# Performance work log

Hardware: AMD Instinct MI355X
Metric: run time of the kernel (lower is better)

The kernel has to match this reference:

```python
import jax, jax.numpy as jnp
import numpy as np

B, N, F, UNITS = 8, 4096, 128, 64
NEG = -1e10
LEAKY_SLOPE = 0.2  # tf.nn.leaky_relu default


def setup_inputs() -> dict:
    key = jax.random.key(0)
    k1, k2, k3, k4, k5 = jax.random.split(key, 5)
    H = jax.random.normal(k1, (B, N, F), dtype=jnp.float32)
    A = jax.random.randint(k2, (B, N, N), 0, 2).astype(jnp.float32)
    # self-loops so every row has at least one unmasked entry
    A = jnp.maximum(A, jnp.eye(N, dtype=jnp.float32)[None])
    W = jax.random.normal(k3, (F, UNITS), dtype=jnp.float32) * (1.0 / np.sqrt(F))
    a_1 = jax.random.normal(k4, (UNITS, 1), dtype=jnp.float32) * (1.0 / np.sqrt(UNITS))
    a_2 = jax.random.normal(k5, (UNITS, 1), dtype=jnp.float32) * (1.0 / np.sqrt(UNITS))
    return {"H": H, "A": A, "W": W, "a_1": a_1, "a_2": a_2}


def reference(H, A, W, a_1, a_2):
    X = H @ W                                  # [B, N, U]
    attn_self = X @ a_1                        # [B, N, 1]
    attn_neigh = X @ a_2                       # [B, N, 1]
    attention = attn_self + jnp.swapaxes(attn_neigh, 1, 2)   # [B, N, N]
    E = jax.nn.leaky_relu(attention, negative_slope=LEAKY_SLOPE)
    masked_E = E + NEG * (1.0 - A)
    alpha = jax.nn.softmax(masked_E, axis=-1)  # row-wise softmax
    H_cap = alpha @ X                          # [B, N, U]
    return jax.nn.relu(H_cap)
```

## Files before the change

kernel.cpp:

```cpp
#include <hip/hip_runtime.h>
#include <hip/hip_bf16.h>


#define NTOK 4096
#define FDIM 128
#define UDIM 64
#define BATCH 8
#define BK 64

typedef __attribute__((ext_vector_type(8))) short short8;
typedef __attribute__((ext_vector_type(4))) float f32x4;

union PackU { unsigned u[4]; short8 s; };

__device__ __forceinline__ unsigned short f2bf(float x) {
    unsigned u = __float_as_uint(x);
    return (unsigned short)((u + 0x7fffu + ((u >> 16) & 1u)) >> 16);
}

__global__ __launch_bounds__(256) void prep_kernel(
    const float* __restrict__ H,
    const float* __restrict__ W,
    const float* __restrict__ a1,
    const float* __restrict__ a2,
    unsigned short* __restrict__ XT,
    float* __restrict__ s_out,
    float* __restrict__ t_out)
{
    __shared__ float Xl[4][16][UDIM + 1];

    const int tid  = threadIdx.x;
    const int wave = tid >> 6, lane = tid & 63;
    const int col  = lane & 15, quad = lane >> 4;
    const int i0   = (blockIdx.x * 4 + wave) * 16;

    f32x4 acc0 = {0,0,0,0}, acc1 = {0,0,0,0}, acc2 = {0,0,0,0}, acc3 = {0,0,0,0};
    const float* hrow = H + (size_t)(i0 + col) * FDIM + quad * 8;

    #pragma unroll
    for (int kb = 0; kb < FDIM; kb += 32) {
        f32x4 h0 = *(const f32x4*)(hrow + kb);
        f32x4 h1 = *(const f32x4*)(hrow + kb + 4);
        short8 afr, b0, b1, b2, b3;
        #pragma unroll
        for (int j = 0; j < 4; ++j) {
            afr[j]     = (short)f2bf(h0[j]);
            afr[4 + j] = (short)f2bf(h1[j]);
        }
        #pragma unroll
        for (int j = 0; j < 8; ++j) {
            int k = kb + quad * 8 + j;
            b0[j] = (short)f2bf(W[k * UDIM + col]);
            b1[j] = (short)f2bf(W[k * UDIM + 16 + col]);
            b2[j] = (short)f2bf(W[k * UDIM + 32 + col]);
            b3[j] = (short)f2bf(W[k * UDIM + 48 + col]);
        }
        acc0 = __builtin_amdgcn_mfma_f32_16x16x32_bf16(afr, b0, acc0, 0, 0, 0);
        acc1 = __builtin_amdgcn_mfma_f32_16x16x32_bf16(afr, b1, acc1, 0, 0, 0);
        acc2 = __builtin_amdgcn_mfma_f32_16x16x32_bf16(afr, b2, acc2, 0, 0, 0);
        acc3 = __builtin_amdgcn_mfma_f32_16x16x32_bf16(afr, b3, acc3, 0, 0, 0);
    }
    #pragma unroll
    for (int r = 0; r < 4; ++r) {
        Xl[wave][quad * 4 + r][col]      = acc0[r];
        Xl[wave][quad * 4 + r][16 + col] = acc1[r];
        Xl[wave][quad * 4 + r][32 + col] = acc2[r];
        Xl[wave][quad * 4 + r][48 + col] = acc3[r];
    }
    __syncthreads();

    const int b = i0 >> 12, n0 = i0 & (NTOK - 1);
    float ps = 0.f, pt = 0.f;
    #pragma unroll
    for (int ui = 0; ui < 16; ++ui) {
        int u = quad * 16 + ui;
        float x = Xl[wave][col][u];
        ps = fmaf(x, a1[u], ps);
        pt = fmaf(x, a2[u], pt);
    }
    ps += __shfl_xor(ps, 16, 64); ps += __shfl_xor(ps, 32, 64);
    pt += __shfl_xor(pt, 16, 64); pt += __shfl_xor(pt, 32, 64);
    const float LOG2E = 1.44269504f;
    if (quad == 0) s_out[i0 + col] = ps * LOG2E;
    if (quad == 1) t_out[i0 + col] = pt * LOG2E;

    #pragma unroll
    for (int ui = 0; ui < 16; ++ui) {
        int u = quad * 16 + ui;
        XT[(size_t)(b * UDIM + u) * NTOK + n0 + col] = f2bf(Xl[wave][col][u]);
    }
}

__global__ __launch_bounds__(256) void attn_kernel(
    const float* __restrict__ A,
    const unsigned short* __restrict__ XT,
    const float* __restrict__ s_in,
    const float* __restrict__ t_in,
    float* __restrict__ out)
{
    __shared__ __align__(16) float          As[2][64][BK + 4];
    __shared__ __align__(16) unsigned short Xs[2][64][BK + 8];

    const int tid  = threadIdx.x;
    const int wave = tid >> 6, lane = tid & 63;
    const int col  = lane & 15, quad = lane >> 4;
    const int b    = blockIdx.x & 7;
    const int i0   = (blockIdx.x >> 3) * 64;

    const int arow = tid >> 4, acol = (tid & 15) * 4;
    const int xrow = tid >> 3, xcol = (tid & 7) * 8;
    const float* agp = A + ((size_t)(b * NTOK + i0 + arow)) * NTOK + acol;
    const unsigned short* xgp = XT + ((size_t)(b * UDIM + xrow)) * NTOK + xcol;

    const float s_m = s_in[b * NTOK + i0 + wave * 16 + col];
    const float* tbase = t_in + b * NTOK;

    f32x4 acc[4];
    #pragma unroll
    for (int f = 0; f < 4; ++f) acc[f] = (f32x4){0,0,0,0};
    float den = 0.f;

    f32x4 av[4], xv[2];

    #pragma unroll
    for (int i = 0; i < 4; ++i)
        av[i] = __builtin_nontemporal_load((const f32x4*)(agp + (size_t)i * 16 * NTOK));
    #pragma unroll
    for (int i = 0; i < 2; ++i)
        xv[i] = *(const f32x4*)(xgp + (size_t)i * 32 * NTOK);
    #pragma unroll
    for (int i = 0; i < 4; ++i) *(f32x4*)&As[0][arow + i * 16][acol] = av[i];
    #pragma unroll
    for (int i = 0; i < 2; ++i) *(f32x4*)&Xs[0][xrow + i * 32][xcol] = xv[i];

    for (int c = 0; c < NTOK / BK; ++c) {
        const int buf = c & 1;
        if (c < NTOK / BK - 1) {
            const float* ag = agp + (c + 1) * BK;
            const unsigned short* xg = xgp + (c + 1) * BK;
            #pragma unroll
            for (int i = 0; i < 4; ++i)
                av[i] = __builtin_nontemporal_load((const f32x4*)(ag + (size_t)i * 16 * NTOK));
            #pragma unroll
            for (int i = 0; i < 2; ++i)
                xv[i] = *(const f32x4*)(xg + (size_t)i * 32 * NTOK);
        }
        __syncthreads();

        #pragma unroll
        for (int ks = 0; ks < 2; ++ks) {
            const float* ar = &As[buf][wave * 16 + col][ks * 32 + quad * 8];
            f32x4 a0 = *(const f32x4*)ar;
            f32x4 a1 = *(const f32x4*)(ar + 4);
            const float* tp = tbase + c * BK + ks * 32 + quad * 8;
            f32x4 t0 = *(const f32x4*)tp;
            f32x4 t1 = *(const f32x4*)(tp + 4);

            unsigned uw[8];
            #pragma unroll
            for (int j = 0; j < 4; ++j) {
                float l0 = s_m + t0[j], l1 = s_m + t1[j];
                float e0 = fmaxf(l0, 0.2f * l0);
                float e1 = fmaxf(l1, 0.2f * l1);
                float w0 = __builtin_amdgcn_exp2f(e0) * a0[j];
                float w1 = __builtin_amdgcn_exp2f(e1) * a1[j];
                den += w0 + w1;
                uw[j]     = __float_as_uint(w0) + 0x8000u;
                uw[4 + j] = __float_as_uint(w1) + 0x8000u;
            }
            PackU p;
            p.u[0] = __builtin_amdgcn_perm(uw[1], uw[0], 0x07060302u);
            p.u[1] = __builtin_amdgcn_perm(uw[3], uw[2], 0x07060302u);
            p.u[2] = __builtin_amdgcn_perm(uw[5], uw[4], 0x07060302u);
            p.u[3] = __builtin_amdgcn_perm(uw[7], uw[6], 0x07060302u);

            short8 bf0 = *(const short8*)&Xs[buf][col]     [ks * 32 + quad * 8];
            short8 bf1 = *(const short8*)&Xs[buf][16 + col][ks * 32 + quad * 8];
            short8 bf2 = *(const short8*)&Xs[buf][32 + col][ks * 32 + quad * 8];
            short8 bf3 = *(const short8*)&Xs[buf][48 + col][ks * 32 + quad * 8];

            acc[0] = __builtin_amdgcn_mfma_f32_16x16x32_bf16(p.s, bf0, acc[0], 0, 0, 0);
            acc[1] = __builtin_amdgcn_mfma_f32_16x16x32_bf16(p.s, bf1, acc[1], 0, 0, 0);
            acc[2] = __builtin_amdgcn_mfma_f32_16x16x32_bf16(p.s, bf2, acc[2], 0, 0, 0);
            acc[3] = __builtin_amdgcn_mfma_f32_16x16x32_bf16(p.s, bf3, acc[3], 0, 0, 0);
        }

        if (c < NTOK / BK - 1) {
            const int nb = buf ^ 1;
            #pragma unroll
            for (int i = 0; i < 4; ++i) *(f32x4*)&As[nb][arow + i * 16][acol] = av[i];
            #pragma unroll
            for (int i = 0; i < 2; ++i) *(f32x4*)&Xs[nb][xrow + i * 32][xcol] = xv[i];
        }
    }

    den += __shfl_xor(den, 16, 64);
    den += __shfl_xor(den, 32, 64);
    #pragma unroll
    for (int r = 0; r < 4; ++r) {
        float dd = __shfl(den, quad * 4 + r, 64);
        const int row = i0 + wave * 16 + quad * 4 + r;
        #pragma unroll
        for (int f = 0; f < 4; ++f) {
            float o = fmaxf(acc[f][r] / dd, 0.f);
            __builtin_nontemporal_store(o, &out[(size_t)(b * NTOK + row) * UDIM + f * 16 + col]);
        }
    }
}

extern "C" void kernel_launch(void* const* d_in, const int* in_sizes, int n_in,
                              void* d_out, int out_size, void* d_ws, size_t ws_size,
                              hipStream_t stream) {
    const float* H  = (const float*)d_in[0];
    const float* A  = (const float*)d_in[1];
    const float* W  = (const float*)d_in[2];
    const float* a1 = (const float*)d_in[3];
    const float* a2 = (const float*)d_in[4];
    float* out = (float*)d_out;

    char* ws = (char*)d_ws;
    unsigned short* XT = (unsigned short*)ws;
    size_t off = (size_t)BATCH * UDIM * NTOK * 2;
    float* s = (float*)(ws + off);
    off += (size_t)BATCH * NTOK * 4;
    float* t = (float*)(ws + off);

    prep_kernel<<<512, 256, 0, stream>>>(H, W, a1, a2, XT, s, t);
    attn_kernel<<<512, 256, 0, stream>>>(A, XT, s, t, out);
}
```

Baseline: 702.4 us.

## Stage A, X and t tiles via direct global-to-LDS loads with XOR swizzle

Replaces the register-staged double buffer (global load into VGPRs, then an LDS store) with global_load_lds direct copies into LDS. The LDS tiles switch from padded rows to an XOR-swizzled layout to avoid bank conflicts, and the t vector is now staged through LDS as well. Explicit vmcnt waits and barriers manage the pipeline. This is meant to cut VGPR pressure and LDS store instructions in a kernel bound by streaming A, at the cost of an extra barrier per chunk and the loss of the nontemporal hint on A.

```diff
diff --git a/kernel.cpp b/kernel.cpp
--- a/kernel.cpp
+++ b/kernel.cpp
@@ -7,6 +7,7 @@
 #define UDIM 64
 #define BATCH 8
 #define BK 64
+#define NCHUNK (NTOK / BK)
 
 typedef __attribute__((ext_vector_type(8))) short short8;
 typedef __attribute__((ext_vector_type(4))) float f32x4;
@@ -16,6 +17,17 @@
 __device__ __forceinline__ unsigned short f2bf(float x) {
     unsigned u = __float_as_uint(x);
     return (unsigned short)((u + 0x7fffu + ((u >> 16) & 1u)) >> 16);
+}
+
+__device__ __forceinline__ void gl2lds16(const void* g, void* l) {
+    __builtin_amdgcn_global_load_lds(
+        (const __attribute__((address_space(1))) unsigned int*)g,
+        (__attribute__((address_space(3))) unsigned int*)l, 16, 0, 0);
+}
+__device__ __forceinline__ void gl2lds4(const void* g, void* l) {
+    __builtin_amdgcn_global_load_lds(
+        (const __attribute__((address_space(1))) unsigned int*)g,
+        (__attribute__((address_space(3))) unsigned int*)l, 4, 0, 0);
 }
 
 __global__ __launch_bounds__(256) void prep_kernel(
@@ -98,8 +110,9 @@
     const float* __restrict__ t_in,
     float* __restrict__ out)
 {
-    __shared__ __align__(16) float          As[2][64][BK + 4];
-    __shared__ __align__(16) unsigned short Xs[2][64][BK + 8];
+    __shared__ __align__(16) float          As[2][64 * BK];
+    __shared__ __align__(16) unsigned short Xs[2][64 * BK];
+    __shared__ __align__(16) float          Ts[2][4][BK];
 
     const int tid  = threadIdx.x;
     const int wave = tid >> 6, lane = tid & 63;
@@ -107,54 +120,66 @@
     const int b    = blockIdx.x & 7;
     const int i0   = (blockIdx.x >> 3) * 64;
 
-    const int arow = tid >> 4, acol = (tid & 15) * 4;
-    const int xrow = tid >> 3, xcol = (tid & 7) * 8;
-    const float* agp = A + ((size_t)(b * NTOK + i0 + arow)) * NTOK + acol;
-    const unsigned short* xgp = XT + ((size_t)(b * UDIM + xrow)) * NTOK + xcol;
+    const float* agp[4];
+    #pragma unroll
+    for (int j = 0; j < 4; ++j) {
+        int r = wave * 16 + j * 4 + (lane >> 4);
+        int v = (lane & 15) ^ (r & 7);
+        agp[j] = A + ((size_t)(b * NTOK + i0 + r)) * NTOK + v * 4;
+    }
+    const unsigned short* xgp[2];
+    #pragma unroll
+    for (int j = 0; j < 2; ++j) {
+        int u = wave * 16 + j * 8 + (lane >> 3);
+        int v = (lane & 7) ^ (u & 7);
+        xgp[j] = XT + ((size_t)(b * UDIM + u)) * NTOK + v * 8;
+    }
+    const float* tgp = t_in + b * NTOK + lane;
 
     const float s_m = s_in[b * NTOK + i0 + wave * 16 + col];
-    const float* tbase = t_in + b * NTOK;
 
     f32x4 acc[4];
     #pragma unroll
     for (int f = 0; f < 4; ++f) acc[f] = (f32x4){0,0,0,0};
     float den = 0.f;
 
-    f32x4 av[4], xv[2];
-
-    #pragma unroll
-    for (int i = 0; i < 4; ++i)
-        av[i] = __builtin_nontemporal_load((const f32x4*)(agp + (size_t)i * 16 * NTOK));
-    #pragma unroll
-    for (int i = 0; i < 2; ++i)
-        xv[i] = *(const f32x4*)(xgp + (size_t)i * 32 * NTOK);
-    #pragma unroll
-    for (int i = 0; i < 4; ++i) *(f32x4*)&As[0][arow + i * 16][acol] = av[i];
-    #pragma unroll
-    for (int i = 0; i < 2; ++i) *(f32x4*)&Xs[0][xrow + i * 32][xcol] = xv[i];
-
-    for (int c = 0; c < NTOK / BK; ++c) {
+    #define STAGE(bufi, cc) do {                                              \
+        gl2lds16(agp[0] + (cc) * BK, (void*)&As[bufi][(wave * 4 + 0) * 256]); \
+        gl2lds16(agp[1] + (cc) * BK, (void*)&As[bufi][(wave * 4 + 1) * 256]); \
+        gl2lds16(agp[2] + (cc) * BK, (void*)&As[bufi][(wave * 4 + 2) * 256]); \
+        gl2lds16(agp[3] + (cc) * BK, (void*)&As[bufi][(wave * 4 + 3) * 256]); \
+        gl2lds16(xgp[0] + (cc) * BK, (void*)&Xs[bufi][(wave * 2 + 0) * 512]); \
+        gl2lds16(xgp[1] + (cc) * BK, (void*)&Xs[bufi][(wave * 2 + 1) * 512]); \
+        gl2lds4 (tgp    + (cc) * BK, (void*)&Ts[bufi][wave][0]);              \
+    } while (0)
+
+    STAGE(0, 0);
+    asm volatile("s_waitcnt vmcnt(0)" ::: "memory");
+    __builtin_amdgcn_s_barrier();
+    __builtin_amdgcn_sched_barrier(0);
+
+    #pragma unroll 2
+    for (int c = 0; c < NCHUNK; ++c) {
         const int buf = c & 1;
-        if (c < NTOK / BK - 1) {
-            const float* ag = agp + (c + 1) * BK;
-            const unsigned short* xg = xgp + (c + 1) * BK;
-            #pragma unroll
-            for (int i = 0; i < 4; ++i)
-                av[i] = __builtin_nontemporal_load((const f32x4*)(ag + (size_t)i * 16 * NTOK));
-            #pragma unroll
-            for (int i = 0; i < 2; ++i)
-                xv[i] = *(const f32x4*)(xg + (size_t)i * 32 * NTOK);
-        }
-        __syncthreads();
-
+        if (c + 1 < NCHUNK) {
+            STAGE(buf ^ 1, c + 1);
+            asm volatile("s_waitcnt vmcnt(7)" ::: "memory");
+        } else {
+            asm volatile("s_waitcnt vmcnt(0)" ::: "memory");
+        }
+        __builtin_amdgcn_sched_barrier(0);
+        __builtin_amdgcn_s_barrier();
+        __builtin_amdgcn_sched_barrier(0);
+
+        const int R   = wave * 16 + col;
+        const int xsw = col & 7;
         #pragma unroll
         for (int ks = 0; ks < 2; ++ks) {
-            const float* ar = &As[buf][wave * 16 + col][ks * 32 + quad * 8];
-            f32x4 a0 = *(const f32x4*)ar;
-            f32x4 a1 = *(const f32x4*)(ar + 4);
-            const float* tp = tbase + c * BK + ks * 32 + quad * 8;
-            f32x4 t0 = *(const f32x4*)tp;
-            f32x4 t1 = *(const f32x4*)(tp + 4);
+            const int v0 = 8 * ks + 2 * quad;
+            f32x4 a0 = *(const f32x4*)&As[buf][R * 64 + ((v0)     ^ (R & 7)) * 4];
+            f32x4 a1 = *(const f32x4*)&As[buf][R * 64 + ((v0 + 1) ^ (R & 7)) * 4];
+            f32x4 t0 = *(const f32x4*)&Ts[buf][wave][ks * 32 + quad * 8];
+            f32x4 t1 = *(const f32x4*)&Ts[buf][wave][ks * 32 + quad * 8 + 4];
 
             unsigned uw[8];
             #pragma unroll
@@ -174,25 +199,22 @@
             p.u[2] = __builtin_amdgcn_perm(uw[5], uw[4], 0x07060302u);
             p.u[3] = __builtin_amdgcn_perm(uw[7], uw[6], 0x07060302u);
 
-            short8 bf0 = *(const short8*)&Xs[buf][col]     [ks * 32 + quad * 8];
-            short8 bf1 = *(const short8*)&Xs[buf][16 + col][ks * 32 + quad * 8];
-            short8 bf2 = *(const short8*)&Xs[buf][32 + col][ks * 32 + quad * 8];
-            short8 bf3 = *(const short8*)&Xs[buf][48 + col][ks * 32 + quad * 8];
+            const int xv = (4 * ks + quad) ^ xsw;
+            short8 bf0 = *(const short8*)&Xs[buf][(col)      * 64 + xv * 8];
+            short8 bf1 = *(const short8*)&Xs[buf][(16 + col) * 64 + xv * 8];
+            short8 bf2 = *(const short8*)&Xs[buf][(32 + col) * 64 + xv * 8];
+            short8 bf3 = *(const short8*)&Xs[buf][(48 + col) * 64 + xv * 8];
 
             acc[0] = __builtin_amdgcn_mfma_f32_16x16x32_bf16(p.s, bf0, acc[0], 0, 0, 0);
             acc[1] = __builtin_amdgcn_mfma_f32_16x16x32_bf16(p.s, bf1, acc[1], 0, 0, 0);
             acc[2] = __builtin_amdgcn_mfma_f32_16x16x32_bf16(p.s, bf2, acc[2], 0, 0, 0);
             acc[3] = __builtin_amdgcn_mfma_f32_16x16x32_bf16(p.s, bf3, acc[3], 0, 0, 0);
         }
-
-        if (c < NTOK / BK - 1) {
-            const int nb = buf ^ 1;
-            #pragma unroll
-            for (int i = 0; i < 4; ++i) *(f32x4*)&As[nb][arow + i * 16][acol] = av[i];
-            #pragma unroll
-            for (int i = 0; i < 2; ++i) *(f32x4*)&Xs[nb][xrow + i * 32][xcol] = xv[i];
-        }
-    }
+        __builtin_amdgcn_sched_barrier(0);
+        __builtin_amdgcn_s_barrier();
+        __builtin_amdgcn_sched_barrier(0);
+    }
+    #undef STAGE
 
     den += __shfl_xor(den, 16, 64);
     den += __shfl_xor(den, 32, 64);
```

After: 719.9 us. +2.5%, slower.

## Restructure attention kernel: stage bf16 weights in LDS, split K across waves

Applied to the files above, without the earlier changes.

The attention kernel now uses 512-thread blocks over 32 rows. Each wave streams 4 full rows of A with wide coalesced loads, computes the masked exp weights once, and stores them as bf16 in a double-buffered LDS tile of 512 columns. The MFMA step reads X directly from global/L2 instead of staging it in LDS, and splits the K dimension across four wave groups, with a final LDS reduction and a per-row denominator reduction through shuffles. The aim is better coalescing of the dominant A stream, fewer barriers per byte, and more blocks in flight. In exchange, each block re-reads X from cache and adds a cross-wave reduction.

```diff
diff --git a/kernel.cpp b/kernel.cpp
--- a/kernel.cpp
+++ b/kernel.cpp
@@ -6,7 +6,8 @@
 #define FDIM 128
 #define UDIM 64
 #define BATCH 8
-#define BK 64
+#define CK 512
+#define NCH (NTOK / CK)
 
 typedef __attribute__((ext_vector_type(8))) short short8;
 typedef __attribute__((ext_vector_type(4))) float f32x4;
@@ -91,120 +92,143 @@
     }
 }
 
-__global__ __launch_bounds__(256) void attn_kernel(
+__global__ __launch_bounds__(512, 4) void attn_kernel(
     const float* __restrict__ A,
     const unsigned short* __restrict__ XT,
     const float* __restrict__ s_in,
     const float* __restrict__ t_in,
     float* __restrict__ out)
 {
-    __shared__ __align__(16) float          As[2][64][BK + 4];
-    __shared__ __align__(16) unsigned short Xs[2][64][BK + 8];
+    __shared__ __align__(16) unsigned short Ws[2][32][CK + 8];
+    __shared__ float denl[32];
 
     const int tid  = threadIdx.x;
     const int wave = tid >> 6, lane = tid & 63;
     const int col  = lane & 15, quad = lane >> 4;
     const int b    = blockIdx.x & 7;
-    const int i0   = (blockIdx.x >> 3) * 64;
-
-    const int arow = tid >> 4, acol = (tid & 15) * 4;
-    const int xrow = tid >> 3, xcol = (tid & 7) * 8;
-    const float* agp = A + ((size_t)(b * NTOK + i0 + arow)) * NTOK + acol;
-    const unsigned short* xgp = XT + ((size_t)(b * UDIM + xrow)) * NTOK + xcol;
-
-    const float s_m = s_in[b * NTOK + i0 + wave * 16 + col];
-    const float* tbase = t_in + b * NTOK;
+    const int i0   = (blockIdx.x >> 3) * 32;
+
+    const int g = wave & 1, h = wave >> 1;
+    const int r0 = wave * 4;
+
+    const float* ab = A + ((size_t)(b * NTOK + i0 + r0)) * NTOK + lane * 8;
+    const float* tb = t_in + b * NTOK + lane * 8;
+    float s_r[4];
+    #pragma unroll
+    for (int rr = 0; rr < 4; ++rr) s_r[rr] = s_in[b * NTOK + i0 + r0 + rr];
+
+    const unsigned short* xp[4];
+    #pragma unroll
+    for (int f = 0; f < 4; ++f)
+        xp[f] = XT + ((size_t)(b * UDIM + f * 16 + col)) * NTOK + h * 128 + quad * 8;
 
     f32x4 acc[4];
     #pragma unroll
     for (int f = 0; f < 4; ++f) acc[f] = (f32x4){0,0,0,0};
-    float den = 0.f;
-
-    f32x4 av[4], xv[2];
-
-    #pragma unroll
-    for (int i = 0; i < 4; ++i)
-        av[i] = __builtin_nontemporal_load((const f32x4*)(agp + (size_t)i * 16 * NTOK));
-    #pragma unroll
-    for (int i = 0; i < 2; ++i)
-        xv[i] = *(const f32x4*)(xgp + (size_t)i * 32 * NTOK);
-    #pragma unroll
-    for (int i = 0; i < 4; ++i) *(f32x4*)&As[0][arow + i * 16][acol] = av[i];
-    #pragma unroll
-    for (int i = 0; i < 2; ++i) *(f32x4*)&Xs[0][xrow + i * 32][xcol] = xv[i];
-
-    for (int c = 0; c < NTOK / BK; ++c) {
+    float den_a[4] = {0.f, 0.f, 0.f, 0.f};
+
+    f32x4 av0[4], av1[4], tv0, tv1;
+
+    #define SLOAD(cc) do {                                                         \
+        tv0 = *(const f32x4*)(tb + (cc) * CK);                                     \
+        tv1 = *(const f32x4*)(tb + (cc) * CK + 4);                                 \
+        _Pragma("unroll")                                                          \
+        for (int rr = 0; rr < 4; ++rr) {                                           \
+            av0[rr] = __builtin_nontemporal_load(                                  \
+                (const f32x4*)(ab + (size_t)rr * NTOK + (cc) * CK));               \
+            av1[rr] = __builtin_nontemporal_load(                                  \
+                (const f32x4*)(ab + (size_t)rr * NTOK + (cc) * CK + 4));           \
+        }                                                                          \
+    } while (0)
+
+    #define SWRITE(bufi) do {                                                      \
+        _Pragma("unroll")                                                          \
+        for (int rr = 0; rr < 4; ++rr) {                                           \
+            unsigned uw[8];                                                        \
+            float ds = 0.f;                                                        \
+            _Pragma("unroll")                                                      \
+            for (int j = 0; j < 4; ++j) {                                          \
+                float l0 = s_r[rr] + tv0[j], l1 = s_r[rr] + tv1[j];                \
+                float e0 = fmaxf(l0, 0.2f * l0);               \
+                float e1 = fmaxf(l1, 0.2f * l1);                                   \
+                float w0 = __builtin_amdgcn_exp2f(e0) * av0[rr][j];                \
+                float w1 = __builtin_amdgcn_exp2f(e1) * av1[rr][j];                \
+                ds += w0 + w1;                                                     \
+                uw[j]     = __float_as_uint(w0) + 0x8000u;                         \
+                uw[4 + j] = __float_as_uint(w1) + 0x8000u;                         \
+            }                                                                      \
+            den_a[rr] += ds;                                                       \
+            PackU p;                                                               \
+            p.u[0] = __builtin_amdgcn_perm(uw[1], uw[0], 0x07060302u);             \
+            p.u[1] = __builtin_amdgcn_perm(uw[3], uw[2], 0x07060302u);             \
+            p.u[2] = __builtin_amdgcn_perm(uw[5], uw[4], 0x07060302u);             \
+            p.u[3] = __builtin_amdgcn_perm(uw[7], uw[6], 0x07060302u);             \
+            *(short8*)&Ws[bufi][r0 + rr][lane * 8] = p.s;                          \
+        }                                                                          \
+    } while (0)
+
+    SLOAD(0);
+    SWRITE(0);
+    __syncthreads();
+
+    for (int c = 0; c < NCH; ++c) {
         const int buf = c & 1;
-        if (c < NTOK / BK - 1) {
-            const float* ag = agp + (c + 1) * BK;
-            const unsigned short* xg = xgp + (c + 1) * BK;
+        if (c + 1 < NCH) SLOAD(c + 1);
+
+        const unsigned short* wrow = &Ws[buf][g * 16 + col][h * 128 + quad * 8];
+        #pragma unroll
+        for (int ks = 0; ks < 4; ++ks) {
+            short8 af = *(const short8*)(wrow + ks * 32);
+            short8 b0 = *(const short8*)(xp[0] + c * CK + ks * 32);
+            short8 b1 = *(const short8*)(xp[1] + c * CK + ks * 32);
+            short8 b2 = *(const short8*)(xp[2] + c * CK + ks * 32);
+            short8 b3 = *(const short8*)(xp[3] + c * CK + ks * 32);
+            acc[0] = __builtin_amdgcn_mfma_f32_16x16x32_bf16(af, b0, acc[0], 0, 0, 0);
+            acc[1] = __builtin_amdgcn_mfma_f32_16x16x32_bf16(af, b1, acc[1], 0, 0, 0);
+            acc[2] = __builtin_amdgcn_mfma_f32_16x16x32_bf16(af, b2, acc[2], 0, 0, 0);
+            acc[3] = __builtin_amdgcn_mfma_f32_16x16x32_bf16(af, b3, acc[3], 0, 0, 0);
+        }
+
+        if (c + 1 < NCH) SWRITE(buf ^ 1);
+        __syncthreads();
+    }
+    #undef SLOAD
+    #undef SWRITE
+
+    #pragma unroll
+    for (int rr = 0; rr < 4; ++rr) {
+        float v = den_a[rr];
+        v += __shfl_xor(v, 1, 64);  v += __shfl_xor(v, 2, 64);
+        v += __shfl_xor(v, 4, 64);  v += __shfl_xor(v, 8, 64);
+        v += __shfl_xor(v, 16, 64); v += __shfl_xor(v, 32, 64);
+        if (lane == 0) denl[r0 + rr] = v;
+    }
+    __syncthreads();
+
+    float* red = (float*)&Ws[0][0][0];
+    if (h > 0) {
+        #pragma unroll
+        for (int f = 0; f < 4; ++f)
             #pragma unroll
-            for (int i = 0; i < 4; ++i)
-                av[i] = __builtin_nontemporal_load((const f32x4*)(ag + (size_t)i * 16 * NTOK));
+            for (int r = 0; r < 4; ++r)
+                red[(((h - 1) * 2 + g) * 16 + quad * 4 + r) * 68 + f * 16 + col] = acc[f][r];
+    }
+    __syncthreads();
+    if (h == 0) {
+        #pragma unroll
+        for (int f = 0; f < 4; ++f)
             #pragma unroll
-            for (int i = 0; i < 2; ++i)
-                xv[i] = *(const f32x4*)(xg + (size_t)i * 32 * NTOK);
-        }
-        __syncthreads();
-
-        #pragma unroll
-        for (int ks = 0; ks < 2; ++ks) {
-            const float* ar = &As[buf][wave * 16 + col][ks * 32 + quad * 8];
-            f32x4 a0 = *(const f32x4*)ar;
-            f32x4 a1 = *(const f32x4*)(ar + 4);
-            const float* tp = tbase + c * BK + ks * 32 + quad * 8;
-            f32x4 t0 = *(const f32x4*)tp;
-            f32x4 t1 = *(const f32x4*)(tp + 4);
-
-            unsigned uw[8];
-            #pragma unroll
-            for (int j = 0; j < 4; ++j) {
-                float l0 = s_m + t0[j], l1 = s_m + t1[j];
-                float e0 = fmaxf(l0, 0.2f * l0);
-                float e1 = fmaxf(l1, 0.2f * l1);
-                float w0 = __builtin_amdgcn_exp2f(e0) * a0[j];
-                float w1 = __builtin_amdgcn_exp2f(e1) * a1[j];
-                den += w0 + w1;
-                uw[j]     = __float_as_uint(w0) + 0x8000u;
-                uw[4 + j] = __float_as_uint(w1) + 0x8000u;
+            for (int r = 0; r < 4; ++r) {
+                const int rl = quad * 4 + r;
+                float v = acc[f][r]
+                        + red[((0 * 2 + g) * 16 + rl) * 68 + f * 16 + col]
+                        + red[((1 * 2 + g) * 16 + rl) * 68 + f * 16 + col]
+                        + red[((2 * 2 + g) * 16 + rl) * 68 + f * 16 + col];
+                float dd = denl[g * 16 + rl];
+                float o  = fmaxf(v / dd, 0.f);
+                __builtin_nontemporal_store(
+                    o, &out[(size_t)(b * NTOK + i0 + g * 16 + rl) * UDIM + f * 16 + col]);
             }
-            PackU p;
-            p.u[0] = __builtin_amdgcn_perm(uw[1], uw[0], 0x07060302u);
-            p.u[1] = __builtin_amdgcn_perm(uw[3], uw[2], 0x07060302u);
-            p.u[2] = __builtin_amdgcn_perm(uw[5], uw[4], 0x07060302u);
-            p.u[3] = __builtin_amdgcn_perm(uw[7], uw[6], 0x07060302u);
-
-            short8 bf0 = *(const short8*)&Xs[buf][col]     [ks * 32 + quad * 8];
-            short8 bf1 = *(const short8*)&Xs[buf][16 + col][ks * 32 + quad * 8];
-            short8 bf2 = *(const short8*)&Xs[buf][32 + col][ks * 32 + quad * 8];
-            short8 bf3 = *(const short8*)&Xs[buf][48 + col][ks * 32 + quad * 8];
-
-            acc[0] = __builtin_amdgcn_mfma_f32_16x16x32_bf16(p.s, bf0, acc[0], 0, 0, 0);
-            acc[1] = __builtin_amdgcn_mfma_f32_16x16x32_bf16(p.s, bf1, acc[1], 0, 0, 0);
-            acc[2] = __builtin_amdgcn_mfma_f32_16x16x32_bf16(p.s, bf2, acc[2], 0, 0, 0);
-            acc[3] = __builtin_amdgcn_mfma_f32_16x16x32_bf16(p.s, bf3, acc[3], 0, 0, 0);
-        }
-
-        if (c < NTOK / BK - 1) {
-            const int nb = buf ^ 1;
-            #pragma unroll
-            for (int i = 0; i < 4; ++i) *(f32x4*)&As[nb][arow + i * 16][acol] = av[i];
-            #pragma unroll
-            for (int i = 0; i < 2; ++i) *(f32x4*)&Xs[nb][xrow + i * 32][xcol] = xv[i];
-        }
-    }
-
-    den += __shfl_xor(den, 16, 64);
-    den += __shfl_xor(den, 32, 64);
-    #pragma unroll
-    for (int r = 0; r < 4; ++r) {
-        float dd = __shfl(den, quad * 4 + r, 64);
-        const int row = i0 + wave * 16 + quad * 4 + r;
-        #pragma unroll
-        for (int f = 0; f < 4; ++f) {
-            float o = fmaxf(acc[f][r] / dd, 0.f);
-            __builtin_nontemporal_store(o, &out[(size_t)(b * NTOK + row) * UDIM + f * 16 + col]);
-        }
     }
 }
 
@@ -226,5 +250,5 @@
     float* t = (float*)(ws + off);
 
     prep_kernel<<<512, 256, 0, stream>>>(H, W, a1, a2, XT, s, t);
-    attn_kernel<<<512, 256, 0, stream>>>(A, XT, s, t, out);
-}
+    attn_kernel<<<1024, 512, 0, stream>>>(A, XT, s, t, out);
+}
```

New measurement: 783.0 us. 11.5% more time.
